# Kernel tuning notes

Measured on AMD Instinct MI355X. Metric: run time of the kernel, lower is better.

Reference implementation:

```python
import jax, jax.numpy as jnp
import numpy as np

HIDDEN = 1024
NUM_SLOTS = 8
VOCAB = 32768
B, T = 32, 2048


def setup_inputs() -> dict:
    key = jax.random.key(0)
    k1, k2, k3 = jax.random.split(key, 3)
    hidden_states = jax.random.normal(k1, (B, T, HIDDEN), dtype=jnp.float32)
    attention_mask = jnp.ones((B, T), dtype=jnp.int32)
    # slot projector weight, torch Linear stores [out, in] = [H*num_slots, H]
    W_proj = jax.random.normal(k2, (HIDDEN * NUM_SLOTS, HIDDEN), dtype=jnp.float32) * 0.02
    codebook = jax.random.normal(k3, (VOCAB, HIDDEN), dtype=jnp.float32) * 0.02
    return {"hidden_states": hidden_states, "attention_mask": attention_mask,
            "W_proj": W_proj, "codebook": codebook}


def _masked_mean(states, mask):
    # states [B,T,H], mask [B,T] -> [B,H]
    w = mask.astype(states.dtype)
    denom = jnp.clip(w.sum(axis=1, keepdims=True), 1.0)
    return jnp.einsum('bth,bt->bh', states, w) / denom


def reference(hidden_states, attention_mask, W_proj, codebook):
    pooled = _masked_mean(hidden_states, attention_mask)          # [B,H]
    pre_q = (pooled @ W_proj.T).reshape(-1, NUM_SLOTS, HIDDEN)    # [B,S,H]
    distances = (jnp.sum(pre_q ** 2, axis=-1, keepdims=True)
                 - 2.0 * jnp.einsum('bsh,vh->bsv', pre_q, codebook)
                 + jnp.sum(codebook ** 2, axis=-1)[None, None, :])  # [B,S,V]
    logits = -distances
    indices = jnp.argmax(logits, axis=-1)                         # [B,S]
    embedded = codebook[indices]                                  # [B,S,H]
    quantized = pre_q + jax.lax.stop_gradient(embedded - pre_q)
    commitment_loss = jnp.mean((pre_q - jax.lax.stop_gradient(embedded)) ** 2)
    codebook_loss = jnp.mean((embedded - jax.lax.stop_gradient(pre_q)) ** 2)
    return logits, indices, pre_q, quantized, commitment_loss, codebook_loss
```

## Files before the change

### kernel.cpp

```cpp
#include <hip/hip_runtime.h>
#include <hip/hip_bf16.h>

#define B_ 32
#define T_ 2048
#define H_ 1024
#define S_ 8
#define V_ 32768
#define ROWS 256
#define OUTO 8192
#define NCHUNK 64
#define TCHUNK 32
#define NCB 256
#define DELTA2 0.008f
#define MAXCAND 512

typedef __attribute__((ext_vector_type(8))) short s16x8;
typedef __attribute__((ext_vector_type(8))) unsigned short u16x8;
typedef __attribute__((ext_vector_type(4))) float f32x4;

__device__ __forceinline__ unsigned short bf16hi(float x) {
  return __builtin_bit_cast(unsigned short, __float2bfloat16(x));
}

__global__ void pool_kernel(const float* __restrict__ hidden,
                            const int* __restrict__ mask,
                            float* __restrict__ part_pool,
                            int* __restrict__ cntpart) {
  int b = blockIdx.x;
  int chunk = blockIdx.y;
  int t0 = chunk * TCHUNK;
  int h4 = threadIdx.x * 4;
  const float* base = hidden + ((size_t)b * T_ + t0) * H_ + h4;
  const int* mrow = mask + (size_t)b * T_ + t0;
  float a0 = 0.f, a1 = 0.f, a2 = 0.f, a3 = 0.f;
  int mcount = 0;
#pragma unroll 4
  for (int i = 0; i < TCHUNK; ++i) {
    int mi = mrow[i];
    float m = (float)mi;
    mcount += mi;
    float4 v = *reinterpret_cast<const float4*>(base + (size_t)i * H_);
    a0 += m * v.x; a1 += m * v.y; a2 += m * v.z; a3 += m * v.w;
  }
  float* pp = part_pool + ((size_t)chunk * B_ + b) * H_ + h4;
  *reinterpret_cast<float4*>(pp) = make_float4(a0, a1, a2, a3);
  if (threadIdx.x == 0) cntpart[chunk * B_ + b] = mcount;
}

__global__ void pool_reduce_kernel(const float* __restrict__ part_pool,
                                   const int* __restrict__ cntpart,
                                   float* __restrict__ pooledT,
                                   int* __restrict__ cnt) {
  int g = blockIdx.x * 256 + threadIdx.x;
  float s = 0.f;
  for (int c = 0; c < NCHUNK; ++c) s += part_pool[(size_t)c * (H_ * B_) + g];
  int b = g >> 10, h = g & 1023;
  pooledT[h * B_ + b] = s;
  if (g < B_) {
    int cs = 0;
    for (int c = 0; c < NCHUNK; ++c) cs += cntpart[c * B_ + g];
    cnt[g] = cs;
  }
}

__global__ __launch_bounds__(256) void proj_kernel(const float* __restrict__ Wp,
                            const float* __restrict__ pooledT,
                            const int* __restrict__ cnt,
                            float* __restrict__ preq) {
  __shared__ float pl[32][260];
  const int t = threadIdx.x;
  const int og = t >> 5, b = t & 31;
  const int o = blockIdx.x * 8 + og;
  const float* wrow = Wp + (size_t)o * H_;
  float acc = 0.f;
  for (int pass = 0; pass < 4; ++pass) {
    int k0 = pass * 256;
    __syncthreads();
#pragma unroll
    for (int i = 0; i < 8; ++i) {
      int f = i * 1024 + t * 4;
      int hl = f >> 5, b4 = f & 31;
      float4 v = *reinterpret_cast<const float4*>(&pooledT[(size_t)(k0 + hl) * 32 + b4]);
      pl[b4 + 0][hl] = v.x; pl[b4 + 1][hl] = v.y;
      pl[b4 + 2][hl] = v.z; pl[b4 + 3][hl] = v.w;
    }
    __syncthreads();
    const float* w0 = wrow + k0;
#pragma unroll 8
    for (int j = 0; j < 64; ++j) {
      float4 p = *reinterpret_cast<const float4*>(&pl[b][4 * j]);
      float4 a = *reinterpret_cast<const float4*>(w0 + 4 * j);
      acc += a.x * p.x + a.y * p.y + a.z * p.z + a.w * p.w;
    }
  }
  float denom = fmaxf((float)cnt[b], 1.0f);
  preq[(size_t)b * OUTO + o] = acc / denom;
}

__global__ void aprep_kernel(const float* __restrict__ preq,
                             unsigned short* __restrict__ A_img,
                             float* __restrict__ xnorm) {
  int row = blockIdx.x;
  int t = threadIdx.x;
  int k0 = 4 * t;
  int ks = k0 >> 5, kk = k0 & 31;
  float4 v = reinterpret_cast<const float4*>(preq + (size_t)row * H_)[t];
  float xv[4] = {v.x, v.y, v.z, v.w};
  unsigned short hv[4];
  float s = 0.f;
#pragma unroll
  for (int i = 0; i < 4; ++i) { s += xv[i] * xv[i]; hv[i] = bf16hi(xv[i]); }
  *reinterpret_cast<ushort4*>(&A_img[(size_t)ks * 8192 + row * 32 + kk]) =
      make_ushort4(hv[0], hv[1], hv[2], hv[3]);
#pragma unroll
  for (int off = 1; off < 64; off <<= 1) s += __shfl_xor(s, off);
  __shared__ float ps[4];
  if ((t & 63) == 0) ps[t >> 6] = s;
  __syncthreads();
  if (t == 0) xnorm[row] = ps[0] + ps[1] + ps[2] + ps[3];
}

__global__ __launch_bounds__(512, 2) void dist_kernel(
    const unsigned short* __restrict__ A_img, const float* __restrict__ codebook,
    const float* __restrict__ xnorm, float* __restrict__ logits,
    float* __restrict__ pscore) {
  __shared__ __align__(16) unsigned short Bs[2][128][40];
  __shared__ float cn[128];
  __shared__ float xns[256];
  __shared__ float bwv[2][256];

  const int t = threadIdx.x;
  const int l = t & 63;
  const int w = t >> 6;
  const int cb = w & 1;
  const int m0 = (w >> 1) * 64;
  const int lr = l & 15, lq = l >> 4;
  const int blk = blockIdx.x;
  const int v0 = blk * 128;

  if (t < 256) xns[t] = xnorm[t];

  const int sn = t >> 2;
  const int sk = (t & 3) * 8;
  const float* cbp = codebook + (size_t)(v0 + sn) * H_ + sk;
  float csq = 0.f;

  f32x4 acc[4][4];
#pragma unroll
  for (int i = 0; i < 4; ++i)
#pragma unroll
    for (int j = 0; j < 4; ++j) acc[i][j] = (f32x4){0.f, 0.f, 0.f, 0.f};

  unsigned int aoff[4];
#pragma unroll
  for (int mt = 0; mt < 4; ++mt)
    aoff[mt] = (unsigned int)((m0 + mt * 16 + lr) * 32 + lq * 8);

#define LOAD_A(DST, KS)                                                           \
  _Pragma("unroll")                                                               \
  for (int mt = 0; mt < 4; ++mt)                                                  \
    DST[mt] = *reinterpret_cast<const s16x8*>(&A_img[(size_t)(KS) * 8192 + aoff[mt]]);

#define CONV(BUF, X0, X1)                                                         \
  {                                                                               \
    float xv[8] = {X0.x, X0.y, X0.z, X0.w, X1.x, X1.y, X1.z, X1.w};               \
    u16x8 hv;                                                                     \
    _Pragma("unroll")                                                             \
    for (int i = 0; i < 8; ++i) { float x = xv[i]; csq += x * x; hv[i] = bf16hi(x); } \
    *reinterpret_cast<u16x8*>(&Bs[BUF][sn][sk]) = hv;                             \
  }

#define BAR()                                                                     \
  asm volatile("s_waitcnt lgkmcnt(0)" ::: "memory");                              \
  __builtin_amdgcn_s_barrier();                                                   \
  __builtin_amdgcn_sched_barrier(0);

#define STEP(KS, AU, AN, CC0, CC1, CL0, CL1)                                      \
  {                                                                               \
    LOAD_A(AN, (KS) + 1);                                                         \
    int kl = (KS) + 3; if (kl > 31) kl = 31;                                      \
    CL0 = *reinterpret_cast<const float4*>(cbp + kl * 32);                        \
    CL1 = *reinterpret_cast<const float4*>(cbp + kl * 32 + 4);                    \
    s16x8 bh[4];                                                                  \
    _Pragma("unroll")                                                             \
    for (int nt = 0; nt < 4; ++nt)                                                \
      bh[nt] = *reinterpret_cast<const s16x8*>(&Bs[(KS) & 1][cb * 64 + nt * 16 + lr][lq * 8]); \
    __builtin_amdgcn_s_setprio(1);                                                \
    _Pragma("unroll")                                                             \
    for (int mt = 0; mt < 4; ++mt)                                                \
      _Pragma("unroll")                                                           \
      for (int nt = 0; nt < 4; ++nt)                                              \
        acc[mt][nt] = __builtin_amdgcn_mfma_f32_16x16x32_bf16(AU[mt], bh[nt], acc[mt][nt], 0, 0, 0); \
    __builtin_amdgcn_s_setprio(0);                                                \
    CONV(((KS) + 1) & 1, CC0, CC1);                                               \
    BAR();                                                                        \
  }

  s16x8 a0[4], a1[4], a2[4];
  LOAD_A(a0, 0);
  float4 c00 = *reinterpret_cast<const float4*>(cbp);
  float4 c01 = *reinterpret_cast<const float4*>(cbp + 4);
  float4 c10 = *reinterpret_cast<const float4*>(cbp + 32);
  float4 c11 = *reinterpret_cast<const float4*>(cbp + 36);
  float4 c20 = *reinterpret_cast<const float4*>(cbp + 64);
  float4 c21 = *reinterpret_cast<const float4*>(cbp + 68);
  CONV(0, c00, c01);
  BAR();

  for (int ks = 0; ks < 30; ks += 3) {
    STEP(ks,     a0, a1, c10, c11, c00, c01);
    STEP(ks + 1, a1, a2, c20, c21, c10, c11);
    STEP(ks + 2, a2, a0, c00, c01, c20, c21);
  }
  {
    LOAD_A(a1, 31);
    s16x8 bh[4];
#pragma unroll
    for (int nt = 0; nt < 4; ++nt)
      bh[nt] = *reinterpret_cast<const s16x8*>(&Bs[0][cb * 64 + nt * 16 + lr][lq * 8]);
    __builtin_amdgcn_s_setprio(1);
#pragma unroll
    for (int mt = 0; mt < 4; ++mt)
#pragma unroll
      for (int nt = 0; nt < 4; ++nt)
        acc[mt][nt] = __builtin_amdgcn_mfma_f32_16x16x32_bf16(a0[mt], bh[nt], acc[mt][nt], 0, 0, 0);
    __builtin_amdgcn_s_setprio(0);
    CONV(1, c10, c11);
    BAR();
  }
  {
    s16x8 bh[4];
#pragma unroll
    for (int nt = 0; nt < 4; ++nt)
      bh[nt] = *reinterpret_cast<const s16x8*>(&Bs[1][cb * 64 + nt * 16 + lr][lq * 8]);
    __builtin_amdgcn_s_setprio(1);
#pragma unroll
    for (int mt = 0; mt < 4; ++mt)
#pragma unroll
      for (int nt = 0; nt < 4; ++nt)
        acc[mt][nt] = __builtin_amdgcn_mfma_f32_16x16x32_bf16(a1[mt], bh[nt], acc[mt][nt], 0, 0, 0);
    __builtin_amdgcn_s_setprio(0);
  }

  csq += __shfl_xor(csq, 1);
  csq += __shfl_xor(csq, 2);
  if ((t & 3) == 0) cn[sn] = csq;
  __syncthreads();

  const float NEG = -3.402823466e38f;
#pragma unroll
  for (int mt = 0; mt < 4; ++mt) {
#pragma unroll
    for (int r = 0; r < 4; ++r) {
      int row = m0 + mt * 16 + lq * 4 + r;
      float xn = xns[row];
      float bs = NEG;
#pragma unroll
      for (int nt = 0; nt < 4; ++nt) {
        int col = cb * 64 + nt * 16 + lr;
        float sc = 2.f * acc[mt][nt][r] - cn[col];
        logits[(size_t)row * V_ + v0 + col] = sc - xn;
        bs = fmaxf(bs, sc);
      }
#pragma unroll
      for (int off = 1; off < 16; off <<= 1) bs = fmaxf(bs, __shfl_xor(bs, off));
      if (lr == 0) bwv[cb][row] = bs;
    }
  }
  __syncthreads();
  if (t < 256) pscore[(size_t)t * NCB + blk] = fmaxf(bwv[0][t], bwv[1][t]);
}

__global__ __launch_bounds__(256) void finalize_kernel(
    const float* __restrict__ preq, const float* __restrict__ codebook,
    const float* __restrict__ logits, const float* __restrict__ xnorm,
    const float* __restrict__ pscore,
    float* __restrict__ out_idx, float* __restrict__ out_quant,
    float* __restrict__ lsum) {
  int row = blockIdx.x;
  int t = threadIdx.x;
  float m = pscore[(size_t)row * NCB + t];
#pragma unroll
  for (int off = 1; off < 64; off <<= 1) m = fmaxf(m, __shfl_xor(m, off));
  __shared__ float wm[4];
  if ((t & 63) == 0) wm[t >> 6] = m;
  __syncthreads();
  float M = fmaxf(fmaxf(wm[0], wm[1]), fmaxf(wm[2], wm[3]));
  float thr = M - xnorm[row] - DELTA2;
  __shared__ int cand[MAXCAND];
  __shared__ int ncand;
  if (t == 0) ncand = 0;
  __syncthreads();
  const float* lrow = logits + (size_t)row * V_;
#pragma unroll 4
  for (int it = 0; it < 32; ++it) {
    int c0 = it * 1024 + t * 4;
    float4 lg = *reinterpret_cast<const float4*>(lrow + c0);
    if (lg.x >= thr) { int p = atomicAdd(&ncand, 1); if (p < MAXCAND) cand[p] = c0; }
    if (lg.y >= thr) { int p = atomicAdd(&ncand, 1); if (p < MAXCAND) cand[p] = c0 + 1; }
    if (lg.z >= thr) { int p = atomicAdd(&ncand, 1); if (p < MAXCAND) cand[p] = c0 + 2; }
    if (lg.w >= thr) { int p = atomicAdd(&ncand, 1); if (p < MAXCAND) cand[p] = c0 + 3; }
  }
  __syncthreads();
  int total = ncand;
  const float* pr = preq + (size_t)row * H_;
  int idx;
  if (total <= MAXCAND) {
    __shared__ double sd[4];
    double best = -1.0e300; int bi = V_;
    for (int j = 0; j < total; ++j) {
      int c = cand[j];
      const float* cr = codebook + (size_t)c * H_;
      float4 cv = reinterpret_cast<const float4*>(cr)[t];
      float4 pv = reinterpret_cast<const float4*>(pr)[t];
      double p = (double)cv.x * (2.0 * (double)pv.x - (double)cv.x)
               + (double)cv.y * (2.0 * (double)pv.y - (double)cv.y)
               + (double)cv.z * (2.0 * (double)pv.z - (double)cv.z)
               + (double)cv.w * (2.0 * (double)pv.w - (double)cv.w);
#pragma unroll
      for (int off = 1; off < 64; off <<= 1) p += __shfl_xor(p, off);
      if ((t & 63) == 0) sd[t >> 6] = p;
      __syncthreads();
      double s = sd[0] + sd[1] + sd[2] + sd[3];
      if (s > best || (s == best && c < bi)) { best = s; bi = c; }
      __syncthreads();
    }
    idx = bi;
  } else {
    double best = -1.0e300; int bi = V_;
    for (int c = t; c < V_; c += 256) {
      const float* cr = codebook + (size_t)c * H_;
      double s = 0.0;
      for (int k = 0; k < H_; k += 4) {
        float4 cv = *reinterpret_cast<const float4*>(cr + k);
        float4 pv = *reinterpret_cast<const float4*>(pr + k);
        s += (double)cv.x * (2.0 * (double)pv.x - (double)cv.x)
           + (double)cv.y * (2.0 * (double)pv.y - (double)cv.y)
           + (double)cv.z * (2.0 * (double)pv.z - (double)cv.z)
           + (double)cv.w * (2.0 * (double)pv.w - (double)cv.w);
      }
      if (s > best || (s == best && c < bi)) { best = s; bi = c; }
    }
#pragma unroll
    for (int off = 1; off < 64; off <<= 1) {
      double os = __shfl_xor(best, off);
      int oi = __shfl_xor(bi, off);
      if (os > best || (os == best && oi < bi)) { best = os; bi = oi; }
    }
    __shared__ double fb[4]; __shared__ int fbi[4];
    if ((t & 63) == 0) { fb[t >> 6] = best; fbi[t >> 6] = bi; }
    __syncthreads();
    double b0 = fb[0]; int i0 = fbi[0];
    for (int wv = 1; wv < 4; ++wv)
      if (fb[wv] > b0 || (fb[wv] == b0 && fbi[wv] < i0)) { b0 = fb[wv]; i0 = fbi[wv]; }
    idx = i0;
  }
  if (t == 0) out_idx[row] = (float)idx;
  float4 e = reinterpret_cast<const float4*>(codebook + (size_t)idx * H_)[t];
  float4 p4 = reinterpret_cast<const float4*>(pr)[t];
  float4 q;
  q.x = p4.x + (e.x - p4.x); q.y = p4.y + (e.y - p4.y);
  q.z = p4.z + (e.z - p4.z); q.w = p4.w + (e.w - p4.w);
  reinterpret_cast<float4*>(out_quant)[row * 256 + t] = q;
  float dx = p4.x - e.x, dy = p4.y - e.y, dz = p4.z - e.z, dw = p4.w - e.w;
  float ls = dx * dx + dy * dy + dz * dz + dw * dw;
#pragma unroll
  for (int off = 1; off < 64; off <<= 1) ls += __shfl_xor(ls, off);
  __shared__ float lss[4];
  if ((t & 63) == 0) lss[t >> 6] = ls;
  __syncthreads();
  if (t == 0) lsum[row] = lss[0] + lss[1] + lss[2] + lss[3];
}

__global__ void loss_kernel(const float* __restrict__ lsum, float* __restrict__ out_loss) {
  int t = threadIdx.x;
  float s = lsum[t];
#pragma unroll
  for (int off = 1; off < 64; off <<= 1) s += __shfl_xor(s, off);
  __shared__ float a[4];
  if ((t & 63) == 0) a[t >> 6] = s;
  __syncthreads();
  if (t == 0) {
    float lv = (a[0] + a[1] + a[2] + a[3]) / (float)(ROWS * H_);
    out_loss[0] = lv; out_loss[1] = lv;
  }
}

extern "C" void kernel_launch(void* const* d_in, const int* in_sizes, int n_in,
                              void* d_out, int out_size, void* d_ws, size_t ws_size,
                              hipStream_t stream) {
  (void)in_sizes; (void)n_in; (void)out_size; (void)ws_size;
  const float* hidden   = (const float*)d_in[0];
  const int* mask       = (const int*)d_in[1];
  const float* Wp       = (const float*)d_in[2];
  const float* codebook = (const float*)d_in[3];

  float* out = (float*)d_out;
  float* out_logits = out;
  float* out_idx    = out + 8388608;
  float* out_preq   = out_idx + 256;
  float* out_quant  = out_preq + 262144;
  float* out_loss   = out_quant + 262144;

  float* part_pool = out_logits;
  int*   cntpart   = (int*)(out_logits + 2097152);
  float* pooledT   = out_logits + 2099200;
  int*   cnt       = (int*)(out_logits + 2131968);

  float* ws     = (float*)d_ws;
  float* xnorm  = ws;
  float* pscore = ws + 256;
  float* lsum   = ws + 65792;
  unsigned short* A_img = (unsigned short*)(ws + 66048);

  pool_kernel<<<dim3(B_, NCHUNK), 256, 0, stream>>>(hidden, mask, part_pool, cntpart);
  pool_reduce_kernel<<<128, 256, 0, stream>>>(part_pool, cntpart, pooledT, cnt);
  proj_kernel<<<1024, 256, 0, stream>>>(Wp, pooledT, cnt, out_preq);
  aprep_kernel<<<ROWS, 256, 0, stream>>>(out_preq, A_img, xnorm);
  dist_kernel<<<NCB, 512, 0, stream>>>(A_img, codebook, xnorm, out_logits, pscore);
  finalize_kernel<<<ROWS, 256, 0, stream>>>(out_preq, codebook, out_logits, xnorm,
                                            pscore, out_idx, out_quant, lsum);
  loss_kernel<<<1, 256, 0, stream>>>(lsum, out_loss);
}
```

Before: 192.8 us.

## Load codebook B-fragments directly into registers, dropping LDS staging and barriers

The dist kernel no longer stages the converted bf16 codebook tile through shared memory with per-step barriers. Each lane now loads its own MFMA B-fragment straight from global memory, converts it in registers, and keeps per-column squared norms locally, reducing them with shuffles. This removes LDS traffic and workgroup synchronisation from the K loop. In exchange, each codebook element is loaded redundantly by the four waves that share a column block, which raises global/L2 traffic and register pressure, and the new loop uses only two-deep register prefetching.

```diff
diff --git a/kernel.cpp b/kernel.cpp
--- a/kernel.cpp
+++ b/kernel.cpp
@@ -124,8 +124,6 @@
     const unsigned short* __restrict__ A_img, const float* __restrict__ codebook,
     const float* __restrict__ xnorm, float* __restrict__ logits,
     float* __restrict__ pscore) {
-  __shared__ __align__(16) unsigned short Bs[2][128][40];
-  __shared__ float cn[128];
   __shared__ float xns[256];
   __shared__ float bwv[2][256];
 
@@ -140,111 +138,87 @@
 
   if (t < 256) xns[t] = xnorm[t];
 
-  const int sn = t >> 2;
-  const int sk = (t & 3) * 8;
-  const float* cbp = codebook + (size_t)(v0 + sn) * H_ + sk;
-  float csq = 0.f;
-
-  f32x4 acc[4][4];
-#pragma unroll
-  for (int i = 0; i < 4; ++i)
-#pragma unroll
-    for (int j = 0; j < 4; ++j) acc[i][j] = (f32x4){0.f, 0.f, 0.f, 0.f};
+  const float* bptr = codebook + (size_t)(v0 + cb * 64 + lr) * H_ + lq * 8;
 
   unsigned int aoff[4];
 #pragma unroll
   for (int mt = 0; mt < 4; ++mt)
     aoff[mt] = (unsigned int)((m0 + mt * 16 + lr) * 32 + lq * 8);
+
+  f32x4 acc[4][4];
+#pragma unroll
+  for (int i = 0; i < 4; ++i)
+#pragma unroll
+    for (int j = 0; j < 4; ++j) acc[i][j] = (f32x4){0.f, 0.f, 0.f, 0.f};
+
+  float csq4[4] = {0.f, 0.f, 0.f, 0.f};
 
 #define LOAD_A(DST, KS)                                                           \
   _Pragma("unroll")                                                               \
   for (int mt = 0; mt < 4; ++mt)                                                  \
     DST[mt] = *reinterpret_cast<const s16x8*>(&A_img[(size_t)(KS) * 8192 + aoff[mt]]);
 
-#define CONV(BUF, X0, X1)                                                         \
-  {                                                                               \
-    float xv[8] = {X0.x, X0.y, X0.z, X0.w, X1.x, X1.y, X1.z, X1.w};               \
+#define LOAD_B(DST, KS)                                                           \
+  _Pragma("unroll")                                                               \
+  for (int nt = 0; nt < 4; ++nt) {                                                \
+    DST[nt][0] = *reinterpret_cast<const float4*>(bptr + (size_t)nt * 16384 + (KS) * 32);      \
+    DST[nt][1] = *reinterpret_cast<const float4*>(bptr + (size_t)nt * 16384 + (KS) * 32 + 4);  \
+  }
+
+#define CONV_B(BB, SRC)                                                           \
+  _Pragma("unroll")                                                               \
+  for (int nt = 0; nt < 4; ++nt) {                                                \
+    float xv[8] = {SRC[nt][0].x, SRC[nt][0].y, SRC[nt][0].z, SRC[nt][0].w,        \
+                   SRC[nt][1].x, SRC[nt][1].y, SRC[nt][1].z, SRC[nt][1].w};       \
     u16x8 hv;                                                                     \
     _Pragma("unroll")                                                             \
-    for (int i = 0; i < 8; ++i) { float x = xv[i]; csq += x * x; hv[i] = bf16hi(x); } \
-    *reinterpret_cast<u16x8*>(&Bs[BUF][sn][sk]) = hv;                             \
-  }
-
-#define BAR()                                                                     \
-  asm volatile("s_waitcnt lgkmcnt(0)" ::: "memory");                              \
-  __builtin_amdgcn_s_barrier();                                                   \
-  __builtin_amdgcn_sched_barrier(0);
-
-#define STEP(KS, AU, AN, CC0, CC1, CL0, CL1)                                      \
-  {                                                                               \
-    LOAD_A(AN, (KS) + 1);                                                         \
-    int kl = (KS) + 3; if (kl > 31) kl = 31;                                      \
-    CL0 = *reinterpret_cast<const float4*>(cbp + kl * 32);                        \
-    CL1 = *reinterpret_cast<const float4*>(cbp + kl * 32 + 4);                    \
-    s16x8 bh[4];                                                                  \
+    for (int i = 0; i < 8; ++i) {                                                 \
+      float x = xv[i];                                                            \
+      csq4[nt] += x * x;                                                          \
+      hv[i] = bf16hi(x);                                                          \
+    }                                                                             \
+    BB[nt] = __builtin_bit_cast(s16x8, hv);                                       \
+  }
+
+#define MFMA16(AU, BB)                                                            \
+  __builtin_amdgcn_s_setprio(1);                                                  \
+  _Pragma("unroll")                                                               \
+  for (int mt = 0; mt < 4; ++mt)                                                  \
     _Pragma("unroll")                                                             \
     for (int nt = 0; nt < 4; ++nt)                                                \
-      bh[nt] = *reinterpret_cast<const s16x8*>(&Bs[(KS) & 1][cb * 64 + nt * 16 + lr][lq * 8]); \
-    __builtin_amdgcn_s_setprio(1);                                                \
-    _Pragma("unroll")                                                             \
-    for (int mt = 0; mt < 4; ++mt)                                                \
-      _Pragma("unroll")                                                           \
-      for (int nt = 0; nt < 4; ++nt)                                              \
-        acc[mt][nt] = __builtin_amdgcn_mfma_f32_16x16x32_bf16(AU[mt], bh[nt], acc[mt][nt], 0, 0, 0); \
-    __builtin_amdgcn_s_setprio(0);                                                \
-    CONV(((KS) + 1) & 1, CC0, CC1);                                               \
-    BAR();                                                                        \
-  }
-
-  s16x8 a0[4], a1[4], a2[4];
-  LOAD_A(a0, 0);
-  float4 c00 = *reinterpret_cast<const float4*>(cbp);
-  float4 c01 = *reinterpret_cast<const float4*>(cbp + 4);
-  float4 c10 = *reinterpret_cast<const float4*>(cbp + 32);
-  float4 c11 = *reinterpret_cast<const float4*>(cbp + 36);
-  float4 c20 = *reinterpret_cast<const float4*>(cbp + 64);
-  float4 c21 = *reinterpret_cast<const float4*>(cbp + 68);
-  CONV(0, c00, c01);
-  BAR();
-
-  for (int ks = 0; ks < 30; ks += 3) {
-    STEP(ks,     a0, a1, c10, c11, c00, c01);
-    STEP(ks + 1, a1, a2, c20, c21, c10, c11);
-    STEP(ks + 2, a2, a0, c00, c01, c20, c21);
+      acc[mt][nt] = __builtin_amdgcn_mfma_f32_16x16x32_bf16(AU[mt], BB[nt], acc[mt][nt], 0, 0, 0); \
+  __builtin_amdgcn_s_setprio(0);
+
+  s16x8 aA[4], aB[4], bbA[4], bbB[4];
+  float4 bfA[4][2], bfB[4][2];
+  LOAD_B(bfA, 0);
+  LOAD_A(aA, 0);
+  CONV_B(bbA, bfA);
+
+#pragma unroll 1
+  for (int ks = 0; ks < 30; ks += 2) {
+    LOAD_B(bfB, ks + 1);
+    LOAD_A(aB, ks + 1);
+    MFMA16(aA, bbA);
+    CONV_B(bbB, bfB);
+    LOAD_B(bfA, ks + 2);
+    LOAD_A(aA, ks + 2);
+    MFMA16(aB, bbB);
+    CONV_B(bbA, bfA);
   }
   {
-    LOAD_A(a1, 31);
-    s16x8 bh[4];
-#pragma unroll
-    for (int nt = 0; nt < 4; ++nt)
-      bh[nt] = *reinterpret_cast<const s16x8*>(&Bs[0][cb * 64 + nt * 16 + lr][lq * 8]);
-    __builtin_amdgcn_s_setprio(1);
-#pragma unroll
-    for (int mt = 0; mt < 4; ++mt)
-#pragma unroll
-      for (int nt = 0; nt < 4; ++nt)
-        acc[mt][nt] = __builtin_amdgcn_mfma_f32_16x16x32_bf16(a0[mt], bh[nt], acc[mt][nt], 0, 0, 0);
-    __builtin_amdgcn_s_setprio(0);
-    CONV(1, c10, c11);
-    BAR();
-  }
-  {
-    s16x8 bh[4];
-#pragma unroll
-    for (int nt = 0; nt < 4; ++nt)
-      bh[nt] = *reinterpret_cast<const s16x8*>(&Bs[1][cb * 64 + nt * 16 + lr][lq * 8]);
-    __builtin_amdgcn_s_setprio(1);
-#pragma unroll
-    for (int mt = 0; mt < 4; ++mt)
-#pragma unroll
-      for (int nt = 0; nt < 4; ++nt)
-        acc[mt][nt] = __builtin_amdgcn_mfma_f32_16x16x32_bf16(a1[mt], bh[nt], acc[mt][nt], 0, 0, 0);
-    __builtin_amdgcn_s_setprio(0);
-  }
-
-  csq += __shfl_xor(csq, 1);
-  csq += __shfl_xor(csq, 2);
-  if ((t & 3) == 0) cn[sn] = csq;
+    LOAD_B(bfB, 31);
+    LOAD_A(aB, 31);
+    MFMA16(aA, bbA);
+    CONV_B(bbB, bfB);
+  }
+  MFMA16(aB, bbB);
+
+#pragma unroll
+  for (int nt = 0; nt < 4; ++nt) {
+    csq4[nt] += __shfl_xor(csq4[nt], 16);
+    csq4[nt] += __shfl_xor(csq4[nt], 32);
+  }
   __syncthreads();
 
   const float NEG = -3.402823466e38f;
@@ -258,7 +232,7 @@
 #pragma unroll
       for (int nt = 0; nt < 4; ++nt) {
         int col = cb * 64 + nt * 16 + lr;
-        float sc = 2.f * acc[mt][nt][r] - cn[col];
+        float sc = 2.f * acc[mt][nt][r] - csq4[nt];
         logits[(size_t)row * V_ + v0 + col] = sc - xn;
         bs = fmaxf(bs, sc);
       }
```

Measured after the change: 222.6 us. 15.4% more time.
